# Performance work log

Hardware: AMD Instinct MI355X
Metric: run time of the kernel (lower is better)

## Reference

```python
import jax, jax.numpy as jnp
import numpy as np

BSZ, D = 64, 65536
N_NODES, N_FEATS, EMBED_DIM = 1024, 256, 256


def setup_inputs() -> dict:
    key = jax.random.key(0)
    k1, k2, k3, k4, k5, k6 = jax.random.split(key, 6)
    flat_inputs = jax.random.normal(k1, (BSZ, D), dtype=jnp.float32)
    node_ids = jax.random.randint(k2, (BSZ, D), 0, N_NODES, dtype=jnp.int64 if jax.config.jax_enable_x64 else jnp.int32)
    feat_ids = jax.random.randint(k3, (BSZ, D), 0, N_FEATS, dtype=jnp.int64 if jax.config.jax_enable_x64 else jnp.int32)
    # Linear(n_feats -> embed_dim): W is (embed_dim, n_feats) like torch, plus bias.
    lim = 1.0 / np.sqrt(N_FEATS)
    W = jax.random.uniform(k4, (EMBED_DIM, N_FEATS), minval=-lim, maxval=lim, dtype=jnp.float32)
    b = jax.random.uniform(k5, (EMBED_DIM,), minval=-lim, maxval=lim, dtype=jnp.float32)
    global_emb = jax.random.normal(k6, (N_NODES, EMBED_DIM), dtype=jnp.float32)
    return {"flat_inputs": flat_inputs, "node_ids": node_ids, "feat_ids": feat_ids,
            "W": W, "b": b, "global_emb": global_emb}


def _expand(vals, node_ids, feat_ids, n_nodes, n_feats):
    # scatter-fill a dense (bsz, n_nodes, n_feats) tensor (zeros elsewhere)
    bsz, d = vals.shape
    batch_ids = jnp.broadcast_to(jnp.arange(bsz)[:, None], (bsz, d))
    out = jnp.zeros((bsz, n_nodes, n_feats), dtype=vals.dtype)
    return out.at[batch_ids.ravel(), node_ids.ravel(), feat_ids.ravel()].set(vals.ravel())


def reference(flat_inputs, node_ids, feat_ids, W, b, global_emb):
    obs_mat = _expand(flat_inputs, node_ids, feat_ids, N_NODES, N_FEATS)
    mask_mat = _expand(jnp.ones_like(flat_inputs), node_ids, feat_ids, N_NODES, N_FEATS)
    obs_counts = mask_mat.sum(-1, keepdims=True)            # (bsz, n_nodes, 1)
    obs_masked = jnp.nan_to_num((obs_mat * mask_mat) / obs_counts)
    missing_node_mask = obs_counts == 0
    # nodewise Linear + global embedding broadcast over batch
    embedded = jnp.einsum('bnf,ef->bne', obs_masked, W) + b + global_emb[None, :, :]
    return embedded, missing_node_mask
```

## Files before the change

### kernel.cpp

```cpp
#include <hip/hip_runtime.h>
#include <hip/hip_bf16.h>

#define BSZ    64
#define DLEN   65536
#define NNODES 1024
#define NFEATS 256
#define EDIM   256
#define NROWS  (BSZ * NNODES)

#define NRANGE  16
#define NBUCKET (BSZ * NRANGE)
#define LCAP    320
#define GCAP    4600
#define WPAD    268
#define HROWS   32

typedef __bf16 bf16x8 __attribute__((ext_vector_type(8)));
typedef float  f32x4  __attribute__((ext_vector_type(4)));

__device__ __forceinline__ unsigned short f2bf(float x) {
  union { float f; unsigned u; } c; c.f = x;
  unsigned r = c.u + 0x7FFFu + ((c.u >> 16) & 1u);
  return (unsigned short)(r >> 16);
}

__global__ __launch_bounds__(256) void wconv_kernel(
    const float* __restrict__ W, unsigned short* __restrict__ Wb,
    unsigned* __restrict__ gcnt) {
  int i = (blockIdx.x * 256 + threadIdx.x) * 4;
  float4 w = *(const float4*)(W + i);
  ushort4 o;
  o.x = f2bf(w.x); o.y = f2bf(w.y); o.z = f2bf(w.z); o.w = f2bf(w.w);
  *(ushort4*)(Wb + i) = o;
  if (blockIdx.x == 0) ((uint4*)gcnt)[threadIdx.x] = make_uint4(0u, 0u, 0u, 0u);
}

__global__ __launch_bounds__(512, 6) void bucket_kernel(
    const float* __restrict__ x, const int* __restrict__ nid,
    const int* __restrict__ fid, unsigned* __restrict__ gcnt,
    uint2* __restrict__ gbuf) {
  __shared__ uint2 lbuf[NRANGE][LCAP];
  __shared__ unsigned lcnt[NRANGE];
  __shared__ unsigned lbase[NRANGE];

  const int t = threadIdx.x;
  if (t < NRANGE) lcnt[t] = 0;
  __syncthreads();

  const int b = blockIdx.x >> 4;
  const int base = blockIdx.x * 4096;

#pragma unroll
  for (int k = 0; k < 2; ++k) {
    int i = base + (k * 512 + t) * 4;
    float4 xv = *(const float4*)(x + i);
    int4   nv = *(const int4*)(nid + i);
    int4   fv = *(const int4*)(fid + i);
    int   nd[4] = {nv.x, nv.y, nv.z, nv.w};
    int   ft[4] = {fv.x, fv.y, fv.z, fv.w};
    float vl[4] = {xv.x, xv.y, xv.z, xv.w};
#pragma unroll
    for (int j = 0; j < 4; ++j) {
      int d = (i + j) & 0xFFFF;
      unsigned pack = (((unsigned)(d + 1)) << 15) | ((unsigned)f2bf(vl[j]) >> 1);
      int r = nd[j] >> 6;
      unsigned row = (unsigned)(nd[j] & 63);
      uint2 rec;
      rec.x = pack;
      rec.y = (row << 16) | (row * WPAD + (unsigned)ft[j]);
      unsigned li = atomicAdd(&lcnt[r], 1u);
      if (li < LCAP) {
        lbuf[r][li] = rec;
      } else {
        unsigned gi = atomicAdd(&gcnt[b * NRANGE + r], 1u);
        if (gi < GCAP) gbuf[(size_t)(b * NRANGE + r) * GCAP + gi] = rec;
      }
    }
  }
  __syncthreads();

  if (t < NRANGE) {
    unsigned n = lcnt[t]; if (n > LCAP) n = LCAP;
    lcnt[t] = n;
    lbase[t] = atomicAdd(&gcnt[b * NRANGE + t], n);
  }
  __syncthreads();

  for (int r = 0; r < NRANGE; ++r) {
    unsigned n  = lcnt[r];
    unsigned bs = lbase[r];
    uint2* dst = gbuf + (size_t)(b * NRANGE + r) * GCAP;
    for (unsigned j = t; j < n; j += 512) {
      unsigned gi = bs + j;
      if (gi < GCAP) dst[gi] = lbuf[r][j];
    }
  }
}

__global__ __launch_bounds__(512, 8) void fused_kernel(
    const unsigned* __restrict__ gcnt, const uint2* __restrict__ gbuf,
    const unsigned short* __restrict__ Wb, const float* __restrict__ bias,
    const float* __restrict__ gemb,
    float* __restrict__ out_emb, float* __restrict__ out_mask) {
  __shared__ __align__(16) unsigned win[HROWS * WPAD];
  __shared__ float scl[HROWS];

  const int t = threadIdx.x;
  const int g = blockIdx.x >> 1;
  const int h = blockIdx.x & 1;
  const int row0 = g * 64 + h * HROWS;
  const int nb = (g & 15) * 64 + h * HROWS;

  uint4* wz = (uint4*)win;
  for (int j = t; j < (HROWS * WPAD) / 4; j += 512) wz[j] = make_uint4(0u, 0u, 0u, 0u);
  __syncthreads();

  int cn = (int)gcnt[g]; if (cn > GCAP) cn = GCAP;
  const uint2* bk = gbuf + (size_t)g * GCAP;
  const uint4* bk4 = (const uint4*)bk;
  const unsigned sub = (unsigned)(h * HROWS * WPAD);
  int np = cn >> 1;
  for (int j = t; j < np; j += 512) {
    uint4 rr = bk4[j];
    if (((rr.y >> 21) & 1u) == (unsigned)h) atomicMax(&win[(rr.y & 0xFFFFu) - sub], rr.x);
    if (((rr.w >> 21) & 1u) == (unsigned)h) atomicMax(&win[(rr.w & 0xFFFFu) - sub], rr.z);
  }
  if ((cn & 1) && t == 0) {
    uint2 rec = bk[cn - 1];
    if (((rec.y >> 21) & 1u) == (unsigned)h) atomicMax(&win[(rec.y & 0xFFFFu) - sub], rec.x);
  }
  __syncthreads();

  {
    const int lr  = t >> 4;
    const int seg = t & 15;
    const uint4* rowp = (const uint4*)&win[lr * WPAD];
    int c = 0;
#pragma unroll
    for (int j = 0; j < 4; ++j) {
      uint4 w = rowp[seg + 16 * j];
      c += (w.x != 0u) + (w.y != 0u) + (w.z != 0u) + (w.w != 0u);
    }
    c += __shfl_down(c, 8, 16);
    c += __shfl_down(c, 4, 16);
    c += __shfl_down(c, 2, 16);
    c += __shfl_down(c, 1, 16);
    if (seg == 0) {
      scl[lr] = c ? 1.0f / (float)c : 0.0f;
      out_mask[row0 + lr] = c ? 0.0f : 1.0f;
    }
  }

  const int wv   = t >> 6;
  const int lane = t & 63;
  const int cl   = lane & 15;
  const int q    = lane >> 4;
  const int col0 = wv * 32;

  f32x4 acc[2][2];
#pragma unroll
  for (int mt = 0; mt < 2; ++mt)
#pragma unroll
    for (int nt = 0; nt < 2; ++nt) acc[mt][nt] = (f32x4)(0.0f);

#pragma unroll
  for (int ks = 0; ks < 8; ++ks) {
    bf16x8 bfr[2];
#pragma unroll
    for (int nt = 0; nt < 2; ++nt) {
      const uint4* wp = (const uint4*)(Wb + (size_t)(col0 + nt * 16 + cl) * NFEATS + ks * 32 + q * 8);
      bfr[nt] = __builtin_bit_cast(bf16x8, *wp);
    }
#pragma unroll
    for (int mt = 0; mt < 2; ++mt) {
      const uint4* ap = (const uint4*)&win[(mt * 16 + cl) * WPAD + ks * 32 + q * 8];
      uint4 lo = ap[0], hi = ap[1];
      uint4 pk;
      pk.x = ((lo.x & 0x7FFFu) << 1) | ((lo.y & 0x7FFFu) << 17);
      pk.y = ((lo.z & 0x7FFFu) << 1) | ((lo.w & 0x7FFFu) << 17);
      pk.z = ((hi.x & 0x7FFFu) << 1) | ((hi.y & 0x7FFFu) << 17);
      pk.w = ((hi.z & 0x7FFFu) << 1) | ((hi.w & 0x7FFFu) << 17);
      bf16x8 afr = __builtin_bit_cast(bf16x8, pk);
#pragma unroll
      for (int nt = 0; nt < 2; ++nt)
        acc[mt][nt] = __builtin_amdgcn_mfma_f32_16x16x32_bf16(afr, bfr[nt], acc[mt][nt], 0, 0, 0);
    }
  }
  __syncthreads();

#pragma unroll
  for (int nt = 0; nt < 2; ++nt) {
    int col = col0 + nt * 16 + cl;
    float bv = bias[col];
#pragma unroll
    for (int mt = 0; mt < 2; ++mt) {
#pragma unroll
      for (int r2 = 0; r2 < 4; ++r2) {
        int row = mt * 16 + q * 4 + r2;
        float o = acc[mt][nt][r2] * scl[row] + bv + gemb[(size_t)(nb + row) * EDIM + col];
        out_emb[(size_t)(row0 + row) * EDIM + col] = o;
      }
    }
  }
}

extern "C" void kernel_launch(void* const* d_in, const int* in_sizes, int n_in,
                              void* d_out, int out_size, void* d_ws, size_t ws_size,
                              hipStream_t stream) {
  const float* x    = (const float*)d_in[0];
  const int*   nid  = (const int*)d_in[1];
  const int*   fid  = (const int*)d_in[2];
  const float* W    = (const float*)d_in[3];
  const float* bias = (const float*)d_in[4];
  const float* gemb = (const float*)d_in[5];

  float* out_emb  = (float*)d_out;
  float* out_mask = out_emb + (size_t)NROWS * EDIM;

  unsigned* gcnt = (unsigned*)d_ws;
  uint2* gbuf = (uint2*)((char*)d_ws + 8192);
  unsigned short* Wb = (unsigned short*)((char*)d_ws + 8192 + (size_t)NBUCKET * GCAP * sizeof(uint2));

  wconv_kernel<<<64, 256, 0, stream>>>(W, Wb, gcnt);
  bucket_kernel<<<(BSZ * DLEN) / 4096, 512, 0, stream>>>(x, nid, fid, gcnt, gbuf);
  fused_kernel<<<NBUCKET * 2, 512, 0, stream>>>(gcnt, gbuf, Wb, bias, gemb, out_emb, out_mask);
}
```

Before: 167.6 us.

## Bucket scatter records per 32-node range so each fused block reads only its rows

Doubles the number of node-range buckets to 32 per batch, so each fused block owns exactly one 32-row bucket instead of two blocks sharing a 64-row bucket and each discarding half the records. The bucket kernel handles smaller chunks with one pass per thread. Its flush is split across wavefronts, each draining four ranges. The fused kernel now issues its three bucket loads before any shared-memory atomicMax, removing the row-half filter and the wasted reads. Bucket capacities are smaller (LCAP 112, GCAP 2304), so an unusually skewed distribution could overflow and silently drop records.

```diff
diff --git a/kernel.cpp b/kernel.cpp
--- a/kernel.cpp
+++ b/kernel.cpp
@@ -8,10 +8,11 @@
 #define EDIM   256
 #define NROWS  (BSZ * NNODES)
 
-#define NRANGE  16
+#define NRANGE  32
 #define NBUCKET (BSZ * NRANGE)
-#define LCAP    320
-#define GCAP    4600
+#define CHUNK   2048
+#define LCAP    112
+#define GCAP    2304
 #define WPAD    268
 #define HROWS   32
 
@@ -32,10 +33,11 @@
   ushort4 o;
   o.x = f2bf(w.x); o.y = f2bf(w.y); o.z = f2bf(w.z); o.w = f2bf(w.w);
   *(ushort4*)(Wb + i) = o;
-  if (blockIdx.x == 0) ((uint4*)gcnt)[threadIdx.x] = make_uint4(0u, 0u, 0u, 0u);
-}
-
-__global__ __launch_bounds__(512, 6) void bucket_kernel(
+  if (blockIdx.x < 2)
+    ((uint4*)gcnt)[blockIdx.x * 256 + threadIdx.x] = make_uint4(0u, 0u, 0u, 0u);
+}
+
+__global__ __launch_bounds__(512, 8) void bucket_kernel(
     const float* __restrict__ x, const int* __restrict__ nid,
     const int* __restrict__ fid, unsigned* __restrict__ gcnt,
     uint2* __restrict__ gbuf) {
@@ -47,34 +49,29 @@
   if (t < NRANGE) lcnt[t] = 0;
   __syncthreads();
 
-  const int b = blockIdx.x >> 4;
-  const int base = blockIdx.x * 4096;
-
-#pragma unroll
-  for (int k = 0; k < 2; ++k) {
-    int i = base + (k * 512 + t) * 4;
-    float4 xv = *(const float4*)(x + i);
-    int4   nv = *(const int4*)(nid + i);
-    int4   fv = *(const int4*)(fid + i);
-    int   nd[4] = {nv.x, nv.y, nv.z, nv.w};
-    int   ft[4] = {fv.x, fv.y, fv.z, fv.w};
-    float vl[4] = {xv.x, xv.y, xv.z, xv.w};
-#pragma unroll
-    for (int j = 0; j < 4; ++j) {
-      int d = (i + j) & 0xFFFF;
-      unsigned pack = (((unsigned)(d + 1)) << 15) | ((unsigned)f2bf(vl[j]) >> 1);
-      int r = nd[j] >> 6;
-      unsigned row = (unsigned)(nd[j] & 63);
-      uint2 rec;
-      rec.x = pack;
-      rec.y = (row << 16) | (row * WPAD + (unsigned)ft[j]);
-      unsigned li = atomicAdd(&lcnt[r], 1u);
-      if (li < LCAP) {
-        lbuf[r][li] = rec;
-      } else {
-        unsigned gi = atomicAdd(&gcnt[b * NRANGE + r], 1u);
-        if (gi < GCAP) gbuf[(size_t)(b * NRANGE + r) * GCAP + gi] = rec;
-      }
+  const int b = blockIdx.x >> 5;
+  const int i = blockIdx.x * CHUNK + t * 4;
+
+  float4 xv = *(const float4*)(x + i);
+  int4   nv = *(const int4*)(nid + i);
+  int4   fv = *(const int4*)(fid + i);
+  int   nd[4] = {nv.x, nv.y, nv.z, nv.w};
+  int   ft[4] = {fv.x, fv.y, fv.z, fv.w};
+  float vl[4] = {xv.x, xv.y, xv.z, xv.w};
+#pragma unroll
+  for (int j = 0; j < 4; ++j) {
+    int d = (i + j) & 0xFFFF;
+    unsigned pack = (((unsigned)(d + 1)) << 15) | ((unsigned)f2bf(vl[j]) >> 1);
+    int r = nd[j] >> 5;
+    uint2 rec;
+    rec.x = pack;
+    rec.y = (unsigned)((nd[j] & 31) * WPAD + ft[j]);
+    unsigned li = atomicAdd(&lcnt[r], 1u);
+    if (li < LCAP) {
+      lbuf[r][li] = rec;
+    } else {
+      unsigned gi = atomicAdd(&gcnt[b * NRANGE + r], 1u);
+      if (gi < GCAP) gbuf[(size_t)(b * NRANGE + r) * GCAP + gi] = rec;
     }
   }
   __syncthreads();
@@ -86,11 +83,14 @@
   }
   __syncthreads();
 
-  for (int r = 0; r < NRANGE; ++r) {
+  const int wv = t >> 6, lane = t & 63;
+#pragma unroll
+  for (int rr = 0; rr < 4; ++rr) {
+    int r = wv * 4 + rr;
     unsigned n  = lcnt[r];
     unsigned bs = lbase[r];
     uint2* dst = gbuf + (size_t)(b * NRANGE + r) * GCAP;
-    for (unsigned j = t; j < n; j += 512) {
+    for (unsigned j = lane; j < n; j += 64) {
       unsigned gi = bs + j;
       if (gi < GCAP) dst[gi] = lbuf[r][j];
     }
@@ -106,10 +106,9 @@
   __shared__ float scl[HROWS];
 
   const int t = threadIdx.x;
-  const int g = blockIdx.x >> 1;
-  const int h = blockIdx.x & 1;
-  const int row0 = g * 64 + h * HROWS;
-  const int nb = (g & 15) * 64 + h * HROWS;
+  const int g = blockIdx.x;
+  const int row0 = g * HROWS;
+  const int nb = (g & 31) * HROWS;
 
   uint4* wz = (uint4*)win;
   for (int j = t; j < (HROWS * WPAD) / 4; j += 512) wz[j] = make_uint4(0u, 0u, 0u, 0u);
@@ -118,16 +117,20 @@
   int cn = (int)gcnt[g]; if (cn > GCAP) cn = GCAP;
   const uint2* bk = gbuf + (size_t)g * GCAP;
   const uint4* bk4 = (const uint4*)bk;
-  const unsigned sub = (unsigned)(h * HROWS * WPAD);
   int np = cn >> 1;
-  for (int j = t; j < np; j += 512) {
-    uint4 rr = bk4[j];
-    if (((rr.y >> 21) & 1u) == (unsigned)h) atomicMax(&win[(rr.y & 0xFFFFu) - sub], rr.x);
-    if (((rr.w >> 21) & 1u) == (unsigned)h) atomicMax(&win[(rr.w & 0xFFFFu) - sub], rr.z);
-  }
-  if ((cn & 1) && t == 0) {
-    uint2 rec = bk[cn - 1];
-    if (((rec.y >> 21) & 1u) == (unsigned)h) atomicMax(&win[(rec.y & 0xFFFFu) - sub], rec.x);
+  {
+    uint4 r0, r1, r2;
+    bool v0 = t < np, v1 = t + 512 < np, v2 = t + 1024 < np;
+    if (v0) r0 = bk4[t];
+    if (v1) r1 = bk4[t + 512];
+    if (v2) r2 = bk4[t + 1024];
+    if (v0) { atomicMax(&win[r0.y], r0.x); atomicMax(&win[r0.w], r0.z); }
+    if (v1) { atomicMax(&win[r1.y], r1.x); atomicMax(&win[r1.w], r1.z); }
+    if (v2) { atomicMax(&win[r2.y], r2.x); atomicMax(&win[r2.w], r2.z); }
+    if ((cn & 1) && t == 0) {
+      uint2 rec = bk[cn - 1];
+      atomicMax(&win[rec.y], rec.x);
+    }
   }
   __syncthreads();
 
@@ -222,6 +225,6 @@
   unsigned short* Wb = (unsigned short*)((char*)d_ws + 8192 + (size_t)NBUCKET * GCAP * sizeof(uint2));
 
   wconv_kernel<<<64, 256, 0, stream>>>(W, Wb, gcnt);
-  bucket_kernel<<<(BSZ * DLEN) / 4096, 512, 0, stream>>>(x, nid, fid, gcnt, gbuf);
-  fused_kernel<<<NBUCKET * 2, 512, 0, stream>>>(gcnt, gbuf, Wb, bias, gemb, out_emb, out_mask);
-}
+  bucket_kernel<<<(BSZ * DLEN) / CHUNK, 512, 0, stream>>>(x, nid, fid, gcnt, gbuf);
+  fused_kernel<<<NBUCKET, 512, 0, stream>>>(gcnt, gbuf, Wb, bias, gemb, out_emb, out_mask);
+}
```

Measured after the change: 159.9 us. -4.6%, faster.
